# Optimization experiments

Hardware: AMD Instinct MI355X
Metric: run time of the kernel (lower is better)

## Reference

```python
import jax, jax.numpy as jnp
import numpy as np

B = 16
H_DIM = 512
N_HEADS = 8
HEAD_DIM = H_DIM // N_HEADS  # 64
EPS = 1e-5
DST_LENS = 256 + 16 * np.arange(B)  # ragged dst sizes, total 6016
SRC_LENS = 512 - 8 * np.arange(B)   # ragged src sizes, total 7232


def _pad_info(lens):
    # gather/scatter indices to move between flat ragged layout and [B, Lmax, D]
    lens = np.asarray(lens)
    off = np.concatenate([[0], np.cumsum(lens)[:-1]])
    gid = np.repeat(np.arange(len(lens)), lens)
    pos = np.arange(int(lens.sum())) - np.repeat(off, lens)
    Lmax = int(lens.max())
    mask = jnp.asarray(np.arange(Lmax)[None, :] < lens[:, None])
    return gid, pos, Lmax, mask


def _bn(x, g, b):
    # BatchNorm1d forward with batch statistics (training-mode normalization)
    m = x.mean(0)
    v = ((x - m) ** 2).mean(0)
    return (x - m) / jnp.sqrt(v + EPS) * g + b


def setup_inputs() -> dict:
    key = jax.random.key(0)
    ks = jax.random.split(key, 20)
    total_src = int(SRC_LENS.sum())
    total_dst = int(DST_LENS.sum())
    w = lambda k, shape: jax.random.normal(k, shape, jnp.float32) * 0.02
    return {
        "src_h": jax.random.normal(ks[0], (total_src, H_DIM), jnp.float32),
        "dst_h": jax.random.normal(ks[1], (total_dst, H_DIM), jnp.float32),
        "src_num_verts": jnp.asarray(SRC_LENS, jnp.int32),
        "dst_num_verts": jnp.asarray(DST_LENS, jnp.int32),
        "Wq": w(ks[2], (H_DIM, H_DIM)), "bq": w(ks[3], (H_DIM,)),
        "Wk": w(ks[4], (H_DIM, H_DIM)), "bk": w(ks[5], (H_DIM,)),
        "Wv": w(ks[6], (H_DIM, H_DIM)), "bv": w(ks[7], (H_DIM,)),
        "Wm": w(ks[8], (H_DIM, H_DIM)), "bm": w(ks[9], (H_DIM,)),
        "W1": w(ks[10], (H_DIM, 2 * H_DIM)), "b1": w(ks[11], (H_DIM,)),
        "g1": jnp.ones((H_DIM,), jnp.float32), "be1": jnp.zeros((H_DIM,), jnp.float32),
        "W2": w(ks[12], (H_DIM, H_DIM)), "b2": w(ks[13], (H_DIM,)),
        "g2": jnp.ones((H_DIM,), jnp.float32), "be2": jnp.zeros((H_DIM,), jnp.float32),
    }


def reference(src_h, dst_h, src_num_verts, dst_num_verts,
              Wq, bq, Wk, bk, Wv, bv, Wm, bm,
              W1, b1, g1, be1, W2, b2, g2, be2):
    s_lens = np.asarray(src_num_verts)
    d_lens = np.asarray(dst_num_verts)
    sg, sp, Ls, smask = _pad_info(s_lens)
    dg, dp, Ld, dmask = _pad_info(d_lens)

    # ragged -> padded [B, L, D]
    src_pad = jnp.zeros((B, Ls, H_DIM), src_h.dtype).at[sg, sp].set(src_h)
    dst_pad = jnp.zeros((B, Ld, H_DIM), dst_h.dtype).at[dg, dp].set(dst_h)

    # Conv1d(k=1) projections; channel c = d*num_heads + h -> reshape (head_dim, n_heads)
    q = (dst_pad @ Wq.T + bq).reshape(B, Ld, HEAD_DIM, N_HEADS)
    k = (src_pad @ Wk.T + bk).reshape(B, Ls, HEAD_DIM, N_HEADS)
    v = (src_pad @ Wv.T + bv).reshape(B, Ls, HEAD_DIM, N_HEADS)

    scores = jnp.einsum('bndh,bmdh->bhnm', q, k) / 8.0  # sqrt(head_dim)=8
    scores = jnp.where(smask[:, None, None, :], scores, -1e9)
    attn = jax.nn.softmax(scores, axis=-1)
    o = jnp.einsum('bhnm,bmdh->bndh', attn, v).reshape(B, Ld, H_DIM)
    o = o @ Wm.T + bm  # merge Conv1d(k=1)

    # padded -> ragged
    h_msg = o[dg, dp]  # [total_dst, h_dim]

    h = dst_h
    x = jnp.concatenate([h, h_msg], axis=-1)
    x = _bn(x @ W1.T + b1, g1, be1)
    x = jax.nn.relu(x)
    x = _bn(x @ W2.T + b2, g2, be2)
    return h + x
```

## Files before the change

kernel.cpp:

```cpp
#include <hip/hip_runtime.h>
#include <hip/hip_bf16.h>

#define H_DIM 512
#define N_HEADS 8
#define HEAD_DIM 64
#define NBATCH 16

typedef __attribute__((ext_vector_type(8))) short short8;
typedef __attribute__((ext_vector_type(4))) float floatx4;

typedef unsigned short us16;

#define SW3(r) ((((r) >> 1) & 3) | (((r) & 1) << 2))

__device__ inline unsigned short f2bf(float f) {
  unsigned int u = __float_as_uint(f);
  unsigned int r = (u + 0x7fffu + ((u >> 16) & 1u)) >> 16;
  return (unsigned short)r;
}

__device__ inline void gld16(const us16* g, us16* l) {
  __builtin_amdgcn_global_load_lds(
      (const __attribute__((address_space(1))) void*)g,
      (__attribute__((address_space(3))) void*)l, 16, 0, 0);
}

__global__ __launch_bounds__(256) void cast_all(
    const float* __restrict__ src_h, const float* __restrict__ dst_h,
    const float* __restrict__ Wq, const float* __restrict__ Wk,
    const float* __restrict__ Wv, const float* __restrict__ W1,
    const float* __restrict__ W2,
    us16* __restrict__ src_bf, us16* __restrict__ dst_bf,
    us16* __restrict__ Wqb, us16* __restrict__ Wkv, us16* __restrict__ Wf,
    us16* __restrict__ W2b, float* __restrict__ st,
    int n_src, int n_dst) {
  if (blockIdx.x == 0) {
    float4 z = make_float4(0.f, 0.f, 0.f, 0.f);
    ((float4*)st)[threadIdx.x] = z;
    ((float4*)st)[threadIdx.x + 256] = z;
  }
  const float* srcs[7] = {src_h, dst_h, Wq, Wk, Wv, W1, W2};
  us16* dsts[7] = {src_bf, dst_bf, Wqb, Wkv, Wkv + 262144, Wf, W2b};
  int ns[7] = {n_src, n_dst, 262144, 262144, 262144, 262144, 262144};
  for (int rg = 0; rg < 7; ++rg) {
    const float* sp = srcs[rg];
    us16* dp = dsts[rg];
    const bool strided = (rg == 5);
    for (int i = ((int)blockIdx.x * 256 + (int)threadIdx.x) * 4; i < ns[rg];
         i += (int)gridDim.x * 256 * 4) {
      int j = strided ? ((i >> 9) * 1024 + (i & 511)) : i;
      float4 v = *(const float4*)(sp + j);
      ushort4 o;
      o.x = f2bf(v.x); o.y = f2bf(v.y); o.z = f2bf(v.z); o.w = f2bf(v.w);
      *(ushort4*)(dp + j) = o;
    }
  }
}

__global__ __launch_bounds__(256) void wprep(
    const float* __restrict__ W1, const float* __restrict__ Wm,
    us16* __restrict__ Wf) {
  __shared__ __align__(16) us16 As[64 * 48];
  __shared__ __align__(16) us16 Bs[64 * 48];
  const int t = threadIdx.x, w = t >> 6, lane = t & 63;
  const int lane15 = lane & 15, quad = lane >> 4;
  const int wm = w >> 1, wn = w & 1;
  const int bn_ = blockIdx.x * 64;
  const int bk = blockIdx.y * 64;
  floatx4 acc[2][2];
#pragma unroll
  for (int a = 0; a < 2; ++a)
#pragma unroll
    for (int c = 0; c < 2; ++c) acc[a][c] = (floatx4){0.f, 0.f, 0.f, 0.f};

  for (int j0 = 0; j0 < 512; j0 += 32) {
    {
      int n = t >> 2, jj0 = (t & 3) * 8;
      const float* rp = W1 + (size_t)(bn_ + n) * 1024 + 512 + j0 + jj0;
      float4 va = *(const float4*)(rp);
      float4 vb = *(const float4*)(rp + 4);
      ushort4 pa, pb;
      pa.x = f2bf(va.x); pa.y = f2bf(va.y); pa.z = f2bf(va.z); pa.w = f2bf(va.w);
      pb.x = f2bf(vb.x); pb.y = f2bf(vb.y); pb.z = f2bf(vb.z); pb.w = f2bf(vb.w);
      *(ushort4*)(As + n * 48 + jj0) = pa;
      *(ushort4*)(As + n * 48 + jj0 + 4) = pb;
    }
    {
      int jj = t >> 3, kc0 = (t & 7) * 8;
      const float* rp = Wm + (size_t)(j0 + jj) * 512 + bk + kc0;
      float4 va = *(const float4*)(rp);
      float4 vb = *(const float4*)(rp + 4);
      float vv[8] = {va.x, va.y, va.z, va.w, vb.x, vb.y, vb.z, vb.w};
#pragma unroll
      for (int e = 0; e < 8; ++e) Bs[(kc0 + e) * 48 + jj] = f2bf(vv[e]);
    }
    __syncthreads();
    short8 a_[2], b_[2];
#pragma unroll
    for (int mt = 0; mt < 2; ++mt)
      a_[mt] = *(const short8*)(As + (wm * 32 + mt * 16 + lane15) * 48 + quad * 8);
#pragma unroll
    for (int nt = 0; nt < 2; ++nt)
      b_[nt] = *(const short8*)(Bs + (wn * 32 + nt * 16 + lane15) * 48 + quad * 8);
#pragma unroll
    for (int mt = 0; mt < 2; ++mt)
#pragma unroll
      for (int nt = 0; nt < 2; ++nt)
        acc[mt][nt] = __builtin_amdgcn_mfma_f32_16x16x32_bf16(
            a_[mt], b_[nt], acc[mt][nt], 0, 0, 0);
    __syncthreads();
  }
#pragma unroll
  for (int mt = 0; mt < 2; ++mt) {
    int n0 = bn_ + wm * 32 + mt * 16 + quad * 4;
#pragma unroll
    for (int nt = 0; nt < 2; ++nt) {
      int k = bk + wn * 32 + nt * 16 + lane15;
#pragma unroll
      for (int r = 0; r < 4; ++r)
        Wf[(size_t)(n0 + r) * 1024 + 512 + k] = f2bf(acc[mt][nt][r]);
    }
  }
}

__global__ __launch_bounds__(64) void b1prep(
    const float* __restrict__ W1, const float* __restrict__ b1,
    const float* __restrict__ bm, float* __restrict__ b1p) {
  const int n = blockIdx.x, lane = threadIdx.x;
  const float* rp = W1 + (size_t)n * 1024 + 512 + lane * 8;
  float4 a0 = *(const float4*)(rp);
  float4 a1 = *(const float4*)(rp + 4);
  float4 c0 = *(const float4*)(bm + lane * 8);
  float4 c1 = *(const float4*)(bm + lane * 8 + 4);
  float s = a0.x * c0.x + a0.y * c0.y + a0.z * c0.z + a0.w * c0.w +
            a1.x * c1.x + a1.y * c1.y + a1.z * c1.z + a1.w * c1.w;
#pragma unroll
  for (int o = 1; o < 64; o <<= 1) s += __shfl_xor(s, o);
  if (lane == 0) b1p[n] = b1[n] + s;
}

__device__ inline void gemm_body(
    const us16* __restrict__ A1, const us16* __restrict__ A2,
    const us16* __restrict__ W,
    const float* __restrict__ bias0, const float* __restrict__ bias1,
    void* __restrict__ C0, void* __restrict__ C1, float* __restrict__ stats,
    int M, int N, int K, int mode, int bx, int by) {
  __shared__ __align__(16) us16 As[64 * 128];
  __shared__ __align__(16) us16 Bs[128 * 128];
  const int t = threadIdx.x, w = t >> 6, lane = t & 63;
  const int lane15 = lane & 15, quad = lane >> 4;
  const int bm = bx * 64, bn = by * 128;
  const int srl = lane >> 4;
  const int sl = lane & 15;

  floatx4 acc[4][2];
#pragma unroll
  for (int a = 0; a < 4; ++a)
#pragma unroll
    for (int c = 0; c < 2; ++c) acc[a][c] = (floatx4){0.f, 0.f, 0.f, 0.f};

  for (int k0 = 0; k0 < K; k0 += 128) {
    const us16* Ab = (k0 < 512) ? A1 : A2;
    const int ka = k0 & 511;
#pragma unroll
    for (int p = 0; p < 4; ++p) {
      int row = w * 16 + p * 4 + srl;
      int kg = sl ^ SW3(row);
      gld16(Ab + (size_t)(bm + row) * 512 + ka + kg * 8, As + (w * 16 + p * 4) * 128);
    }
#pragma unroll
    for (int p = 0; p < 8; ++p) {
      int row = w * 32 + p * 4 + srl;
      int kg = sl ^ SW3(row);
      gld16(W + (size_t)(bn + row) * K + k0 + kg * 8, Bs + (w * 32 + p * 4) * 128);
    }
    __syncthreads();
#pragma unroll
    for (int kk = 0; kk < 4; ++kk) {
      const int g = kk * 4 + quad;
      short8 a_[4], b_[2];
#pragma unroll
      for (int mt = 0; mt < 4; ++mt) {
        int r = mt * 16 + lane15;
        a_[mt] = *(const short8*)(As + r * 128 + (g ^ SW3(r)) * 8);
      }
#pragma unroll
      for (int nt = 0; nt < 2; ++nt) {
        int c = w * 32 + nt * 16 + lane15;
        b_[nt] = *(const short8*)(Bs + c * 128 + (g ^ SW3(c)) * 8);
      }
#pragma unroll
      for (int mt = 0; mt < 4; ++mt)
#pragma unroll
        for (int nt = 0; nt < 2; ++nt)
          acc[mt][nt] = __builtin_amdgcn_mfma_f32_16x16x32_bf16(
              a_[mt], b_[nt], acc[mt][nt], 0, 0, 0);
    }
    __syncthreads();
  }

  if (mode == 0) {
#pragma unroll
    for (int nt = 0; nt < 2; ++nt) {
      int col = bn + w * 32 + nt * 16 + lane15;
      float bv = bias0[col];
      float s = 0.f, qq = 0.f;
#pragma unroll
      for (int mt = 0; mt < 4; ++mt) {
        int row0 = bm + mt * 16 + quad * 4;
#pragma unroll
        for (int r = 0; r < 4; ++r) {
          float val = acc[mt][nt][r] + bv;
          ((float*)C0)[(size_t)(row0 + r) * N + col] = val;
          s += val; qq = fmaf(val, val, qq);
        }
      }
      s += __shfl_xor(s, 16); s += __shfl_xor(s, 32);
      qq += __shfl_xor(qq, 16); qq += __shfl_xor(qq, 32);
      if (quad == 0) {
        atomicAdd(&stats[col], s);
        atomicAdd(&stats[512 + col], qq);
      }
    }
  } else if (mode == 1) {
#pragma unroll
    for (int nt = 0; nt < 2; ++nt) {
      int col = bn + w * 32 + nt * 16 + lane15;
      float bv = bias0[col];
      int hh = col & 7, dd = col >> 3;
#pragma unroll
      for (int mt = 0; mt < 4; ++mt) {
        int row0 = bm + mt * 16 + quad * 4;
#pragma unroll
        for (int r = 0; r < 4; ++r)
          ((us16*)C0)[((size_t)hh * M + row0 + r) * 64 + dd] = f2bf(acc[mt][nt][r] + bv);
      }
    }
  } else {
#pragma unroll
    for (int nt = 0; nt < 2; ++nt) {
      int col = bn + w * 32 + nt * 16 + lane15;
      if (col < 512) {
        float bv = bias0[col];
        int hh = col & 7, dd = col >> 3;
#pragma unroll
        for (int mt = 0; mt < 4; ++mt) {
          int row0 = bm + mt * 16 + quad * 4;
#pragma unroll
          for (int r = 0; r < 4; ++r)
            ((us16*)C0)[((size_t)hh * M + row0 + r) * 64 + dd] = f2bf(acc[mt][nt][r] + bv);
        }
      } else {
        int cv = col - 512;
        float bv = bias1[cv];
        int plane = (cv & 7) * 64 + (cv >> 3);
#pragma unroll
        for (int mt = 0; mt < 4; ++mt) {
          int row0 = bm + mt * 16 + quad * 4;
          ushort4 pk;
          pk.x = f2bf(acc[mt][nt][0] + bv);
          pk.y = f2bf(acc[mt][nt][1] + bv);
          pk.z = f2bf(acc[mt][nt][2] + bv);
          pk.w = f2bf(acc[mt][nt][3] + bv);
          *(ushort4*)((us16*)C1 + (size_t)plane * M + row0) = pk;
        }
      }
    }
  }
}

__global__ __launch_bounds__(256) void gemm_ffn(
    const us16* __restrict__ A1, const us16* __restrict__ A2,
    const us16* __restrict__ W,
    const float* __restrict__ bias0, void* __restrict__ C0,
    float* __restrict__ stats, int M, int K) {
  int by = blockIdx.x & 3, bx = blockIdx.x >> 2;
  gemm_body(A1, A2, W, bias0, nullptr, C0, nullptr, stats, M, 512, K, 0, bx, by);
}

__global__ __launch_bounds__(256) void gemm_qkv(
    const us16* __restrict__ dst_bf, const us16* __restrict__ src_bf,
    const us16* __restrict__ Wqb, const us16* __restrict__ Wkv,
    const float* __restrict__ bq, const float* __restrict__ bk,
    const float* __restrict__ bv,
    us16* __restrict__ Qh, us16* __restrict__ Kh, us16* __restrict__ Vt,
    int Md, int Ms) {
  int i = blockIdx.x;
  int nq = (Md / 64) * 4;
  if (i < nq) {
    gemm_body(dst_bf, dst_bf, Wqb, bq, nullptr, Qh, nullptr, nullptr,
              Md, 512, 512, 1, i >> 2, i & 3);
  } else {
    int j = i - nq;
    gemm_body(src_bf, src_bf, Wkv, bk, bv, Kh, Vt, nullptr,
              Ms, 1024, 512, 4, j >> 3, j & 7);
  }
}

__global__ __launch_bounds__(256) void attn_v6(
    const us16* __restrict__ Qh, const us16* __restrict__ Kh,
    const us16* __restrict__ Vt, const int* __restrict__ dlens,
    const int* __restrict__ slens, us16* __restrict__ O,
    int Md, int Ms) {
  const int b = blockIdx.x, h = blockIdx.y, tile = blockIdx.z;
  int doff = 0, soff = 0;
  for (int i = 0; i < NBATCH; ++i)
    if (i < b) { doff += dlens[i]; soff += slens[i]; }
  const int dlen = dlens[b], slen = slens[b];
  if (tile * 64 >= dlen) return;

  __shared__ __align__(16) us16 Ks[64 * 64];
  __shared__ __align__(16) us16 Vts[64 * 64];
  __shared__ __align__(16) us16 Pw[4][16 * 72];

  const int t = threadIdx.x, wv = t >> 6, lane = t & 63;
  const int lane15 = lane & 15, quad = lane >> 4;
  const int i0w = tile * 64 + wv * 16;
  const bool active = i0w < dlen;

  const us16* Qp = Qh + ((size_t)h * Md + doff + (active ? i0w : 0)) * 64;
  const us16* Kp = Kh + ((size_t)h * Ms + soff) * 64;
  const us16* Vtp = Vt + ((size_t)h * 64) * Ms + soff;

  short8 af0 = *(const short8*)(Qp + (size_t)lane15 * 64 + quad * 8);
  short8 af1 = *(const short8*)(Qp + (size_t)lane15 * 64 + 32 + quad * 8);

  floatx4 oa[4];
#pragma unroll
  for (int nt = 0; nt < 4; ++nt) oa[nt] = (floatx4){0.f, 0.f, 0.f, 0.f};
  float m_r[4] = {-3.0e38f, -3.0e38f, -3.0e38f, -3.0e38f};
  float l_r[4] = {0.f, 0.f, 0.f, 0.f};

  for (int j0 = 0; j0 < slen; j0 += 64) {
#pragma unroll
    for (int p = 0; p < 2; ++p) {
      int row = wv * 16 + p * 8 + (lane >> 3);
      int sl = lane & 7;
      int kg = sl ^ SW3(row);
      gld16(Kp + (size_t)(j0 + row) * 64 + kg * 8, Ks + (wv * 16 + p * 8) * 64);
      gld16(Vtp + (size_t)row * Ms + j0 + kg * 8, Vts + (wv * 16 + p * 8) * 64);
    }
    __syncthreads();

    if (active) {
      floatx4 s[4];
#pragma unroll
      for (int jt = 0; jt < 4; ++jt) {
        int j = jt * 16 + lane15;
        short8 b0 = *(const short8*)(Ks + j * 64 + ((quad ^ SW3(j)) * 8));
        short8 b1 = *(const short8*)(Ks + j * 64 + (((4 + quad) ^ SW3(j)) * 8));
        floatx4 a = (floatx4){0.f, 0.f, 0.f, 0.f};
        a = __builtin_amdgcn_mfma_f32_16x16x32_bf16(af0, b0, a, 0, 0, 0);
        a = __builtin_amdgcn_mfma_f32_16x16x32_bf16(af1, b1, a, 0, 0, 0);
        s[jt] = a;
      }
      float mx[4] = {-3.0e38f, -3.0e38f, -3.0e38f, -3.0e38f};
#pragma unroll
      for (int jt = 0; jt < 4; ++jt) {
        bool valid = (j0 + jt * 16 + lane15) < slen;
#pragma unroll
        for (int r = 0; r < 4; ++r) {
          float v = valid ? s[jt][r] * 0.125f : -3.0e38f;
          s[jt][r] = v;
          mx[r] = fmaxf(mx[r], v);
        }
      }
#pragma unroll
      for (int r = 0; r < 4; ++r) {
        mx[r] = fmaxf(mx[r], __shfl_xor(mx[r], 1));
        mx[r] = fmaxf(mx[r], __shfl_xor(mx[r], 2));
        mx[r] = fmaxf(mx[r], __shfl_xor(mx[r], 4));
        mx[r] = fmaxf(mx[r], __shfl_xor(mx[r], 8));
      }
      float al[4], sum[4];
#pragma unroll
      for (int r = 0; r < 4; ++r) {
        float mn = fmaxf(m_r[r], mx[r]);
        al[r] = __expf(m_r[r] - mn);
        m_r[r] = mn;
        sum[r] = 0.f;
      }
#pragma unroll
      for (int jt = 0; jt < 4; ++jt)
#pragma unroll
        for (int r = 0; r < 4; ++r) {
          float e = __expf(s[jt][r] - m_r[r]);
          sum[r] += e;
          Pw[wv][(quad * 4 + r) * 72 + jt * 16 + lane15] = f2bf(e);
        }
#pragma unroll
      for (int r = 0; r < 4; ++r) {
        sum[r] += __shfl_xor(sum[r], 1);
        sum[r] += __shfl_xor(sum[r], 2);
        sum[r] += __shfl_xor(sum[r], 4);
        sum[r] += __shfl_xor(sum[r], 8);
        l_r[r] = l_r[r] * al[r] + sum[r];
      }
#pragma unroll
      for (int nt = 0; nt < 4; ++nt)
#pragma unroll
        for (int r = 0; r < 4; ++r) oa[nt][r] *= al[r];
      short8 pa0 = *(const short8*)(&Pw[wv][lane15 * 72 + quad * 8]);
      short8 pa1 = *(const short8*)(&Pw[wv][lane15 * 72 + 32 + quad * 8]);
#pragma unroll
      for (int nt = 0; nt < 4; ++nt) {
        int d = nt * 16 + lane15;
        short8 v0 = *(const short8*)(Vts + d * 64 + ((quad ^ SW3(d)) * 8));
        short8 v1 = *(const short8*)(Vts + d * 64 + (((4 + quad) ^ SW3(d)) * 8));
        oa[nt] = __builtin_amdgcn_mfma_f32_16x16x32_bf16(pa0, v0, oa[nt], 0, 0, 0);
        oa[nt] = __builtin_amdgcn_mfma_f32_16x16x32_bf16(pa1, v1, oa[nt], 0, 0, 0);
      }
    }
    __syncthreads();
  }

  if (active) {
    float linv[4];
#pragma unroll
    for (int r = 0; r < 4; ++r) linv[r] = 1.f / l_r[r];
#pragma unroll
    for (int r = 0; r < 4; ++r) {
      int i = quad * 4 + r;
      us16* orow = O + (size_t)(doff + i0w + i) * H_DIM + h;
#pragma unroll
      for (int nt = 0; nt < 4; ++nt) {
        int d = nt * 16 + lane15;
        orow[d * 8] = f2bf(oa[nt][r] * linv[r]);
      }
    }
  }
}

__global__ __launch_bounds__(256) void bn_apply(
    const float* __restrict__ X, const float* __restrict__ stats,
    const float* __restrict__ g, const float* __restrict__ be,
    const float* __restrict__ resid, void* __restrict__ Y,
    int M, float invM, int relu, int out_bf) {
  const size_t total = (size_t)M * H_DIM;
  for (size_t i = (size_t)blockIdx.x * 256 + threadIdx.x; i < total;
       i += (size_t)gridDim.x * 256) {
    int c = (int)(i & (H_DIM - 1));
    float mean = stats[c] * invM;
    float var = fmaf(-mean, mean, stats[H_DIM + c] * invM);
    float x = X[i];
    float y = (x - mean) * rsqrtf(var + 1e-5f) * g[c] + be[c];
    if (relu) y = fmaxf(y, 0.f);
    if (resid) y += resid[i];
    if (out_bf) ((us16*)Y)[i] = f2bf(y);
    else ((float*)Y)[i] = y;
  }
}

extern "C" void kernel_launch(void* const* d_in, const int* in_sizes, int n_in,
                              void* d_out, int out_size, void* d_ws, size_t ws_size,
                              hipStream_t stream) {
  const float* src_h = (const float*)d_in[0];
  const float* dst_h = (const float*)d_in[1];
  const int* s_lens  = (const int*)d_in[2];
  const int* d_lens  = (const int*)d_in[3];
  const float* Wq = (const float*)d_in[4];  const float* bq = (const float*)d_in[5];
  const float* Wk = (const float*)d_in[6];  const float* bk = (const float*)d_in[7];
  const float* Wv = (const float*)d_in[8];  const float* bv = (const float*)d_in[9];
  const float* Wm = (const float*)d_in[10]; const float* bm = (const float*)d_in[11];
  const float* W1 = (const float*)d_in[12]; const float* b1 = (const float*)d_in[13];
  const float* g1 = (const float*)d_in[14]; const float* be1 = (const float*)d_in[15];
  const float* W2 = (const float*)d_in[16]; const float* b2 = (const float*)d_in[17];
  const float* g2 = (const float*)d_in[18]; const float* be2 = (const float*)d_in[19];

  const int total_src = in_sizes[0] / H_DIM;
  const int total_dst = in_sizes[1] / H_DIM;

  char* ws = (char*)d_ws;
  us16* src_bf = (us16*)(ws + 0);
  us16* dst_bf = (us16*)(ws + 7405568);
  us16* wbf    = (us16*)(ws + 13565952);
  float* b1p   = (float*)(ws + 16711680);
  us16* Qh     = (us16*)(ws + 17235968);
  us16* Kh     = (us16*)(ws + 23396352);
  us16* Vt     = (us16*)(ws + 30801920);
  us16* Ob     = (us16*)(ws + 38207488);
  us16* X1bf   = (us16*)(ws + 44367872);
  float* st    = (float*)(ws + 50528256);
  float* X1    = (float*)(ws + 17235968);
  float* X2    = (float*)(ws + 30801920);
  float* st1 = st, *st2 = st + 1024;

  us16* Wqb = wbf;
  us16* Wkv = wbf + 262144;
  us16* Wf  = wbf + 786432;
  us16* W2b = wbf + 1310720;

  const int mbd = total_dst / 64;
  const int mbs = total_src / 64;
  const dim3 blk256(256), blk64(64);

  cast_all<<<dim3(2048), blk256, 0, stream>>>(
      src_h, dst_h, Wq, Wk, Wv, W1, W2,
      src_bf, dst_bf, Wqb, Wkv, Wf, W2b, st,
      total_src * H_DIM, total_dst * H_DIM);

  wprep<<<dim3(8, 8), blk256, 0, stream>>>(W1, Wm, Wf);
  b1prep<<<dim3(512), blk64, 0, stream>>>(W1, b1, bm, b1p);

  gemm_qkv<<<dim3(mbd * 4 + mbs * 8), blk256, 0, stream>>>(
      dst_bf, src_bf, Wqb, Wkv, bq, bk, bv, Qh, Kh, Vt, total_dst, total_src);

  attn_v6<<<dim3(NBATCH, N_HEADS, 8), blk256, 0, stream>>>(
      Qh, Kh, Vt, d_lens, s_lens, Ob, total_dst, total_src);

  gemm_ffn<<<dim3(mbd * 4), blk256, 0, stream>>>(
      dst_bf, Ob, Wf, b1p, X1, st1, total_dst, 1024);

  bn_apply<<<dim3(512), blk256, 0, stream>>>(X1, st1, g1, be1, nullptr, X1bf,
                                             total_dst, 1.f / (float)total_dst, 1, 1);

  gemm_ffn<<<dim3(mbd * 4), blk256, 0, stream>>>(
      X1bf, X1bf, W2b, b2, X2, st2, total_dst, 512);

  bn_apply<<<dim3(512), blk256, 0, stream>>>(X2, st2, g2, be2, dst_h, d_out,
                                             total_dst, 1.f / (float)total_dst, 0, 0);
}
```

Before: 261.5 us.

## Double-buffer GEMM k-tiles and merge prep kernels into one launch

The shared GEMM body now uses 64-wide k tiles in two LDS buffers, so the async global-to-LDS loads for the next tile are issued while MFMAs run on the current one. Total LDS use stays the same, and there is one barrier per k-step instead of two. The weight-cast, Wm-folding and bias-folding prep kernels are merged into a single launch split by block index, which removes two kernel launches. The bias-fold path now uses one thread per output with a serial dot product instead of a wave reduction.

```diff
diff --git a/kernel.cpp b/kernel.cpp
--- a/kernel.cpp
+++ b/kernel.cpp
@@ -25,118 +25,114 @@
       (__attribute__((address_space(3))) void*)l, 16, 0, 0);
 }
 
-__global__ __launch_bounds__(256) void cast_all(
+__global__ __launch_bounds__(256) void prep_all(
     const float* __restrict__ src_h, const float* __restrict__ dst_h,
     const float* __restrict__ Wq, const float* __restrict__ Wk,
     const float* __restrict__ Wv, const float* __restrict__ W1,
-    const float* __restrict__ W2,
+    const float* __restrict__ W2, const float* __restrict__ Wm,
+    const float* __restrict__ b1, const float* __restrict__ bm,
     us16* __restrict__ src_bf, us16* __restrict__ dst_bf,
     us16* __restrict__ Wqb, us16* __restrict__ Wkv, us16* __restrict__ Wf,
-    us16* __restrict__ W2b, float* __restrict__ st,
+    us16* __restrict__ W2b, float* __restrict__ b1p, float* __restrict__ st,
     int n_src, int n_dst) {
-  if (blockIdx.x == 0) {
-    float4 z = make_float4(0.f, 0.f, 0.f, 0.f);
-    ((float4*)st)[threadIdx.x] = z;
-    ((float4*)st)[threadIdx.x + 256] = z;
-  }
-  const float* srcs[7] = {src_h, dst_h, Wq, Wk, Wv, W1, W2};
-  us16* dsts[7] = {src_bf, dst_bf, Wqb, Wkv, Wkv + 262144, Wf, W2b};
-  int ns[7] = {n_src, n_dst, 262144, 262144, 262144, 262144, 262144};
-  for (int rg = 0; rg < 7; ++rg) {
-    const float* sp = srcs[rg];
-    us16* dp = dsts[rg];
-    const bool strided = (rg == 5);
-    for (int i = ((int)blockIdx.x * 256 + (int)threadIdx.x) * 4; i < ns[rg];
-         i += (int)gridDim.x * 256 * 4) {
-      int j = strided ? ((i >> 9) * 1024 + (i & 511)) : i;
-      float4 v = *(const float4*)(sp + j);
-      ushort4 o;
-      o.x = f2bf(v.x); o.y = f2bf(v.y); o.z = f2bf(v.z); o.w = f2bf(v.w);
-      *(ushort4*)(dp + j) = o;
-    }
-  }
-}
-
-__global__ __launch_bounds__(256) void wprep(
-    const float* __restrict__ W1, const float* __restrict__ Wm,
-    us16* __restrict__ Wf) {
   __shared__ __align__(16) us16 As[64 * 48];
   __shared__ __align__(16) us16 Bs[64 * 48];
-  const int t = threadIdx.x, w = t >> 6, lane = t & 63;
-  const int lane15 = lane & 15, quad = lane >> 4;
-  const int wm = w >> 1, wn = w & 1;
-  const int bn_ = blockIdx.x * 64;
-  const int bk = blockIdx.y * 64;
-  floatx4 acc[2][2];
-#pragma unroll
-  for (int a = 0; a < 2; ++a)
-#pragma unroll
-    for (int c = 0; c < 2; ++c) acc[a][c] = (floatx4){0.f, 0.f, 0.f, 0.f};
-
-  for (int j0 = 0; j0 < 512; j0 += 32) {
-    {
-      int n = t >> 2, jj0 = (t & 3) * 8;
-      const float* rp = W1 + (size_t)(bn_ + n) * 1024 + 512 + j0 + jj0;
-      float4 va = *(const float4*)(rp);
-      float4 vb = *(const float4*)(rp + 4);
-      ushort4 pa, pb;
-      pa.x = f2bf(va.x); pa.y = f2bf(va.y); pa.z = f2bf(va.z); pa.w = f2bf(va.w);
-      pb.x = f2bf(vb.x); pb.y = f2bf(vb.y); pb.z = f2bf(vb.z); pb.w = f2bf(vb.w);
-      *(ushort4*)(As + n * 48 + jj0) = pa;
-      *(ushort4*)(As + n * 48 + jj0 + 4) = pb;
-    }
-    {
-      int jj = t >> 3, kc0 = (t & 7) * 8;
-      const float* rp = Wm + (size_t)(j0 + jj) * 512 + bk + kc0;
-      float4 va = *(const float4*)(rp);
-      float4 vb = *(const float4*)(rp + 4);
-      float vv[8] = {va.x, va.y, va.z, va.w, vb.x, vb.y, vb.z, vb.w};
-#pragma unroll
-      for (int e = 0; e < 8; ++e) Bs[(kc0 + e) * 48 + jj] = f2bf(vv[e]);
-    }
-    __syncthreads();
-    short8 a_[2], b_[2];
-#pragma unroll
-    for (int mt = 0; mt < 2; ++mt)
-      a_[mt] = *(const short8*)(As + (wm * 32 + mt * 16 + lane15) * 48 + quad * 8);
-#pragma unroll
-    for (int nt = 0; nt < 2; ++nt)
-      b_[nt] = *(const short8*)(Bs + (wn * 32 + nt * 16 + lane15) * 48 + quad * 8);
-#pragma unroll
-    for (int mt = 0; mt < 2; ++mt)
+  const int blk = blockIdx.x;
+  const int t = threadIdx.x;
+
+  if (blk < 2048) {
+    if (blk == 0) {
+      float4 z = make_float4(0.f, 0.f, 0.f, 0.f);
+      ((float4*)st)[t] = z;
+      ((float4*)st)[t + 256] = z;
+    }
+    const float* srcs[7] = {src_h, dst_h, Wq, Wk, Wv, W1, W2};
+    us16* dsts[7] = {src_bf, dst_bf, Wqb, Wkv, Wkv + 262144, Wf, W2b};
+    int ns[7] = {n_src, n_dst, 262144, 262144, 262144, 262144, 262144};
+    for (int rg = 0; rg < 7; ++rg) {
+      const float* sp = srcs[rg];
+      us16* dp = dsts[rg];
+      const bool strided = (rg == 5);
+      for (int i = (blk * 256 + t) * 4; i < ns[rg]; i += 2048 * 256 * 4) {
+        int j = strided ? ((i >> 9) * 1024 + (i & 511)) : i;
+        float4 v = *(const float4*)(sp + j);
+        ushort4 o;
+        o.x = f2bf(v.x); o.y = f2bf(v.y); o.z = f2bf(v.z); o.w = f2bf(v.w);
+        *(ushort4*)(dp + j) = o;
+      }
+    }
+  } else if (blk < 2112) {
+    const int bx = (blk - 2048) & 7, byk = (blk - 2048) >> 3;
+    const int w = t >> 6, lane = t & 63;
+    const int lane15 = lane & 15, quad = lane >> 4;
+    const int wm = w >> 1, wn = w & 1;
+    const int bn_ = bx * 64, bk = byk * 64;
+    floatx4 acc[2][2];
+#pragma unroll
+    for (int a = 0; a < 2; ++a)
+#pragma unroll
+      for (int c = 0; c < 2; ++c) acc[a][c] = (floatx4){0.f, 0.f, 0.f, 0.f};
+    for (int j0 = 0; j0 < 512; j0 += 32) {
+      {
+        int n = t >> 2, jj0 = (t & 3) * 8;
+        const float* rp = W1 + (size_t)(bn_ + n) * 1024 + 512 + j0 + jj0;
+        float4 va = *(const float4*)(rp);
+        float4 vb = *(const float4*)(rp + 4);
+        ushort4 pa, pb;
+        pa.x = f2bf(va.x); pa.y = f2bf(va.y); pa.z = f2bf(va.z); pa.w = f2bf(va.w);
+        pb.x = f2bf(vb.x); pb.y = f2bf(vb.y); pb.z = f2bf(vb.z); pb.w = f2bf(vb.w);
+        *(ushort4*)(As + n * 48 + jj0) = pa;
+        *(ushort4*)(As + n * 48 + jj0 + 4) = pb;
+      }
+      {
+        int jj = t >> 3, kc0 = (t & 7) * 8;
+        const float* rp = Wm + (size_t)(j0 + jj) * 512 + bk + kc0;
+        float4 va = *(const float4*)(rp);
+        float4 vb = *(const float4*)(rp + 4);
+        float vv[8] = {va.x, va.y, va.z, va.w, vb.x, vb.y, vb.z, vb.w};
+#pragma unroll
+        for (int e = 0; e < 8; ++e) Bs[(kc0 + e) * 48 + jj] = f2bf(vv[e]);
+      }
+      __syncthreads();
+      short8 a_[2], b_[2];
+#pragma unroll
+      for (int mt = 0; mt < 2; ++mt)
+        a_[mt] = *(const short8*)(As + (wm * 32 + mt * 16 + lane15) * 48 + quad * 8);
 #pragma unroll
       for (int nt = 0; nt < 2; ++nt)
-        acc[mt][nt] = __builtin_amdgcn_mfma_f32_16x16x32_bf16(
-            a_[mt], b_[nt], acc[mt][nt], 0, 0, 0);
-    __syncthreads();
-  }
-#pragma unroll
-  for (int mt = 0; mt < 2; ++mt) {
-    int n0 = bn_ + wm * 32 + mt * 16 + quad * 4;
-#pragma unroll
-    for (int nt = 0; nt < 2; ++nt) {
-      int k = bk + wn * 32 + nt * 16 + lane15;
-#pragma unroll
-      for (int r = 0; r < 4; ++r)
-        Wf[(size_t)(n0 + r) * 1024 + 512 + k] = f2bf(acc[mt][nt][r]);
-    }
-  }
-}
-
-__global__ __launch_bounds__(64) void b1prep(
-    const float* __restrict__ W1, const float* __restrict__ b1,
-    const float* __restrict__ bm, float* __restrict__ b1p) {
-  const int n = blockIdx.x, lane = threadIdx.x;
-  const float* rp = W1 + (size_t)n * 1024 + 512 + lane * 8;
-  float4 a0 = *(const float4*)(rp);
-  float4 a1 = *(const float4*)(rp + 4);
-  float4 c0 = *(const float4*)(bm + lane * 8);
-  float4 c1 = *(const float4*)(bm + lane * 8 + 4);
-  float s = a0.x * c0.x + a0.y * c0.y + a0.z * c0.z + a0.w * c0.w +
-            a1.x * c1.x + a1.y * c1.y + a1.z * c1.z + a1.w * c1.w;
-#pragma unroll
-  for (int o = 1; o < 64; o <<= 1) s += __shfl_xor(s, o);
-  if (lane == 0) b1p[n] = b1[n] + s;
+        b_[nt] = *(const short8*)(Bs + (wn * 32 + nt * 16 + lane15) * 48 + quad * 8);
+#pragma unroll
+      for (int mt = 0; mt < 2; ++mt)
+#pragma unroll
+        for (int nt = 0; nt < 2; ++nt)
+          acc[mt][nt] = __builtin_amdgcn_mfma_f32_16x16x32_bf16(
+              a_[mt], b_[nt], acc[mt][nt], 0, 0, 0);
+      __syncthreads();
+    }
+#pragma unroll
+    for (int mt = 0; mt < 2; ++mt) {
+      int n0 = bn_ + wm * 32 + mt * 16 + quad * 4;
+#pragma unroll
+      for (int nt = 0; nt < 2; ++nt) {
+        int k = bk + wn * 32 + nt * 16 + lane15;
+#pragma unroll
+        for (int r = 0; r < 4; ++r)
+          Wf[(size_t)(n0 + r) * 1024 + 512 + k] = f2bf(acc[mt][nt][r]);
+      }
+    }
+  } else {
+    int n = (blk - 2112) * 256 + t;
+    if (n < 512) {
+      const float* rp = W1 + (size_t)n * 1024 + 512;
+      float s = 0.f;
+      for (int j = 0; j < 512; j += 4) {
+        float4 a = *(const float4*)(rp + j);
+        float4 c = *(const float4*)(bm + j);
+        s += a.x * c.x + a.y * c.y + a.z * c.z + a.w * c.w;
+      }
+      b1p[n] = b1[n] + s;
+    }
+  }
 }
 
 __device__ inline void gemm_body(
@@ -145,13 +141,13 @@
     const float* __restrict__ bias0, const float* __restrict__ bias1,
     void* __restrict__ C0, void* __restrict__ C1, float* __restrict__ stats,
     int M, int N, int K, int mode, int bx, int by) {
-  __shared__ __align__(16) us16 As[64 * 128];
-  __shared__ __align__(16) us16 Bs[128 * 128];
+  __shared__ __align__(16) us16 As[2 * 64 * 64];
+  __shared__ __align__(16) us16 Bs[2 * 128 * 64];
   const int t = threadIdx.x, w = t >> 6, lane = t & 63;
   const int lane15 = lane & 15, quad = lane >> 4;
   const int bm = bx * 64, bn = by * 128;
-  const int srl = lane >> 4;
-  const int sl = lane & 15;
+  const int lrow = lane >> 3;
+  const int sl = lane & 7;
 
   floatx4 acc[4][2];
 #pragma unroll
@@ -159,35 +155,49 @@
 #pragma unroll
     for (int c = 0; c < 2; ++c) acc[a][c] = (floatx4){0.f, 0.f, 0.f, 0.f};
 
-  for (int k0 = 0; k0 < K; k0 += 128) {
-    const us16* Ab = (k0 < 512) ? A1 : A2;
-    const int ka = k0 & 511;
-#pragma unroll
-    for (int p = 0; p < 4; ++p) {
-      int row = w * 16 + p * 4 + srl;
-      int kg = sl ^ SW3(row);
-      gld16(Ab + (size_t)(bm + row) * 512 + ka + kg * 8, As + (w * 16 + p * 4) * 128);
-    }
-#pragma unroll
-    for (int p = 0; p < 8; ++p) {
-      int row = w * 32 + p * 4 + srl;
-      int kg = sl ^ SW3(row);
-      gld16(W + (size_t)(bn + row) * K + k0 + kg * 8, Bs + (w * 32 + p * 4) * 128);
-    }
-    __syncthreads();
-#pragma unroll
-    for (int kk = 0; kk < 4; ++kk) {
-      const int g = kk * 4 + quad;
+  const int nk = K >> 6;
+
+#define ISSUE(i, b)                                                          \
+  {                                                                          \
+    int k0 = (i) << 6;                                                       \
+    const us16* Ab = (k0 < 512) ? A1 : A2;                                   \
+    int ka = k0 & 511;                                                       \
+    _Pragma("unroll")                                                        \
+    for (int p = 0; p < 2; ++p) {                                            \
+      int rbase = p * 32 + w * 8;                                            \
+      int row = rbase + lrow;                                                \
+      int kg = sl ^ SW3(row);                                                \
+      gld16(Ab + (size_t)(bm + row) * 512 + ka + kg * 8,                     \
+            As + (b) * 4096 + rbase * 64);                                   \
+    }                                                                        \
+    _Pragma("unroll")                                                        \
+    for (int p = 0; p < 4; ++p) {                                            \
+      int rbase = p * 32 + w * 8;                                            \
+      int row = rbase + lrow;                                                \
+      int kg = sl ^ SW3(row);                                                \
+      gld16(W + (size_t)(bn + row) * K + k0 + kg * 8,                        \
+            Bs + (b) * 8192 + rbase * 64);                                   \
+    }                                                                        \
+  }
+
+  ISSUE(0, 0);
+  __syncthreads();
+  for (int i = 0; i < nk; ++i) {
+    const int cur = i & 1;
+    if (i + 1 < nk) ISSUE(i + 1, cur ^ 1);
+#pragma unroll
+    for (int kh = 0; kh < 2; ++kh) {
+      const int g = kh * 4 + quad;
       short8 a_[4], b_[2];
 #pragma unroll
       for (int mt = 0; mt < 4; ++mt) {
         int r = mt * 16 + lane15;
-        a_[mt] = *(const short8*)(As + r * 128 + (g ^ SW3(r)) * 8);
+        a_[mt] = *(const short8*)(As + cur * 4096 + r * 64 + (g ^ SW3(r)) * 8);
       }
 #pragma unroll
       for (int nt = 0; nt < 2; ++nt) {
         int c = w * 32 + nt * 16 + lane15;
-        b_[nt] = *(const short8*)(Bs + c * 128 + (g ^ SW3(c)) * 8);
+        b_[nt] = *(const short8*)(Bs + cur * 8192 + c * 64 + (g ^ SW3(c)) * 8);
       }
 #pragma unroll
       for (int mt = 0; mt < 4; ++mt)
@@ -198,6 +208,7 @@
     }
     __syncthreads();
   }
+#undef ISSUE
 
   if (mode == 0) {
 #pragma unroll
@@ -274,8 +285,8 @@
     const us16* __restrict__ W,
     const float* __restrict__ bias0, void* __restrict__ C0,
     float* __restrict__ stats, int M, int K) {
-  int by = blockIdx.x & 3, bx = blockIdx.x >> 2;
-  gemm_body(A1, A2, W, bias0, nullptr, C0, nullptr, stats, M, 512, K, 0, bx, by);
+  gemm_body(A1, A2, W, bias0, nullptr, C0, nullptr, stats, M, 512, K, 0,
+            blockIdx.x >> 2, blockIdx.x & 3);
 }
 
 __global__ __launch_bounds__(256) void gemm_qkv(
@@ -492,15 +503,12 @@
 
   const int mbd = total_dst / 64;
   const int mbs = total_src / 64;
-  const dim3 blk256(256), blk64(64);
-
-  cast_all<<<dim3(2048), blk256, 0, stream>>>(
-      src_h, dst_h, Wq, Wk, Wv, W1, W2,
-      src_bf, dst_bf, Wqb, Wkv, Wf, W2b, st,
+  const dim3 blk256(256);
+
+  prep_all<<<dim3(2114), blk256, 0, stream>>>(
+      src_h, dst_h, Wq, Wk, Wv, W1, W2, Wm, b1, bm,
+      src_bf, dst_bf, Wqb, Wkv, Wf, W2b, b1p, st,
       total_src * H_DIM, total_dst * H_DIM);
-
-  wprep<<<dim3(8, 8), blk256, 0, stream>>>(W1, Wm, Wf);
-  b1prep<<<dim3(512), blk64, 0, stream>>>(W1, b1, bm, b1p);
 
   gemm_qkv<<<dim3(mbd * 4 + mbs * 8), blk256, 0, stream>>>(
       dst_bf, src_bf, Wqb, Wkv, bq, bk, bv, Qh, Kh, Vt, total_dst, total_src);
```

Result: no change. 258.2 us (-1.3%).
